# Kernel tuning notes

Hardware: AMD Instinct MI355X
Metric: run time of the kernel (lower is better)

## Reference

```python
import jax, jax.numpy as jnp
import numpy as np

B, H, W = 8, 256, 256
NF = 64          # num_feat
E = 12           # num_expert
D = NF * 4       # token dim = 256
CD = D * E       # expanded dim = 3072


def _lrelu(x):
    return jnp.where(x >= 0, x, 0.2 * x)


def _conv(x, w, stride, pad):
    return jax.lax.conv_general_dilated(
        x, w, (stride, stride), [(pad, pad), (pad, pad)],
        dimension_numbers=('NCHW', 'OIHW', 'NCHW'))


def _bn(x, g, b):
    # training-mode BatchNorm2d: batch statistics over (N, H, W)
    m = jnp.mean(x, axis=(0, 2, 3), keepdims=True)
    v = jnp.var(x, axis=(0, 2, 3), keepdims=True)
    xn = (x - m) * jax.lax.rsqrt(v + 1e-5)
    return xn * g[None, :, None, None] + b[None, :, None, None]


def setup_inputs() -> dict:
    key = jax.random.key(0)
    ks = jax.random.split(key, 16)
    s = 0.05
    d = {}
    d['x'] = jax.random.normal(ks[0], (B, 3, H, W), jnp.float32)
    d['conv0_w'] = jax.random.normal(ks[1], (NF, 3, 3, 3)) * s
    d['conv0_b'] = jnp.zeros((NF,))
    d['conv1_w'] = jax.random.normal(ks[2], (NF, NF, 4, 4)) * s
    d['bn1_g'] = jnp.ones((NF,)); d['bn1_b'] = jnp.zeros((NF,))
    d['conv2_w'] = jax.random.normal(ks[3], (2 * NF, NF, 3, 3)) * s
    d['bn2_g'] = jnp.ones((2 * NF,)); d['bn2_b'] = jnp.zeros((2 * NF,))
    d['conv3_w'] = jax.random.normal(ks[4], (2 * NF, 2 * NF, 4, 4)) * s
    d['bn3_g'] = jnp.ones((2 * NF,)); d['bn3_b'] = jnp.zeros((2 * NF,))
    d['conv4_w'] = jax.random.normal(ks[5], (4 * NF, 2 * NF, 3, 3)) * s
    d['bn4_g'] = jnp.ones((4 * NF,)); d['bn4_b'] = jnp.zeros((4 * NF,))
    d['conv5_w'] = jax.random.normal(ks[6], (4 * NF, 4 * NF, 3, 3)) * s
    d['bn5_g'] = jnp.ones((4 * NF,)); d['bn5_b'] = jnp.zeros((4 * NF,))
    d['conv6_w'] = jax.random.normal(ks[7], (4 * NF, 4 * NF, 3, 3)) * s
    d['bn6_g'] = jnp.ones((4 * NF,)); d['bn6_b'] = jnp.zeros((4 * NF,))
    d['w_gating'] = jax.random.normal(ks[8], (D, E))          # torch.randn init
    d['body_w'] = jax.random.normal(ks[9], (D, CD)) * s       # Linear(c_dim, c_dim*blocks)
    d['body_b'] = jnp.zeros((CD,))
    d['ortho_w'] = jax.random.normal(ks[10], (1, 1, CD))      # OrthorTransform weight
    d['cls_w1'] = jax.random.normal(ks[11], (D, NF // 2)) * s # shared classifier
    d['cls_b1'] = jnp.zeros((NF // 2,))
    d['cls_w2'] = jax.random.normal(ks[12], (NF // 2, 1)) * s
    d['cls_b2'] = jnp.zeros((1,))
    return d


def reference(x, conv0_w, conv0_b, conv1_w, bn1_g, bn1_b, conv2_w, bn2_g, bn2_b,
              conv3_w, bn3_g, bn3_b, conv4_w, bn4_g, bn4_b, conv5_w, bn5_g, bn5_b,
              conv6_w, bn6_g, bn6_b, w_gating, body_w, body_b, ortho_w,
              cls_w1, cls_b1, cls_w2, cls_b2):
    # --- FE conv stack ---
    h = _lrelu(_conv(x, conv0_w, 1, 1) + conv0_b[None, :, None, None])
    h = _lrelu(_bn(_conv(h, conv1_w, 2, 1), bn1_g, bn1_b))
    h = _lrelu(_bn(_conv(h, conv2_w, 1, 1), bn2_g, bn2_b))
    h = _lrelu(_bn(_conv(h, conv3_w, 2, 1), bn3_g, bn3_b))
    h = _lrelu(_bn(_conv(h, conv4_w, 1, 1), bn4_g, bn4_b))
    h = _lrelu(_bn(_conv(h, conv5_w, 1, 1), bn5_g, bn5_b))
    h = _lrelu(_bn(_conv(h, conv6_w, 1, 1), bn6_g, bn6_b))
    b, c, hh, ww = h.shape
    tok = h.reshape(b, c, hh * ww).transpose(0, 2, 1)            # (B, N, D)
    # --- softmax router ---
    routing = jax.nn.softmax(jnp.einsum('bnd,de->bne', tok, w_gating), axis=-1)
    # --- CodeReduction: Linear + lrelu, OrthorTransform multiply, lrelu ---
    feat = _lrelu(tok @ body_w + body_b)                         # (B, N, E*D)
    feat = _lrelu(feat * ortho_w)
    feat = feat.reshape(b, hh * ww, E, D)                        # torch.split chunks
    # --- shared expert MLP on every chunk (all classifiers alias one module) ---
    hid = _lrelu(jnp.einsum('bned,df->bnef', feat, cls_w1) + cls_b1)
    outs = (jnp.einsum('bnef,fo->bneo', hid, cls_w2) + cls_b2)[..., 0]  # (B,N,E)
    # --- top-1 select (equivalent to the torch.where cascade) ---
    idx = jnp.argmax(routing, axis=-1, keepdims=True)
    output = jnp.take_along_axis(outs, idx, axis=-1)             # (B, N, 1)
    return output
```

## Files before the change

### kernel.cpp

```cpp
#include <hip/hip_runtime.h>

__device__ __forceinline__ float lrelu(float x) { return x >= 0.f ? x : 0.2f * x; }

typedef const __attribute__((address_space(1))) void* gas_ptr;
typedef __attribute__((address_space(3))) void* las_ptr;

__global__ __launch_bounds__(256) void conv0_k(const float* __restrict__ x,
                                               const float* __restrict__ w,
                                               const float* __restrict__ bias,
                                               float* __restrict__ out) {
    __shared__ float sIn[3][34][34];
    __shared__ float sW[27][16];
    const int H = 256;
    int tid = threadIdx.x, tx = tid & 31, ty = tid >> 5;
    int tX = (blockIdx.x & 7) * 32, tY = (blockIdx.x >> 3) * 32;
    int b = blockIdx.y, cog = blockIdx.z * 16;
    float acc[4][16] = {};
    const float* inB = x + (size_t)b * 3 * H * H;
    for (int idx = tid; idx < 3 * 1156; idx += 256) {
        int ci = idx / 1156, r = idx % 1156, iy = r / 34, ix = r % 34;
        int gy = tY - 1 + iy, gx = tX - 1 + ix;
        float v = 0.f;
        if ((unsigned)gy < 256u && (unsigned)gx < 256u)
            v = inB[(ci * H + gy) * H + gx];
        sIn[ci][iy][ix] = v;
    }
    for (int idx = tid; idx < 27 * 16; idx += 256) {
        int co = idx & 15, rest = idx >> 4;
        sW[rest][co] = w[(cog + co) * 27 + rest];
    }
    __syncthreads();
#pragma unroll
    for (int ci = 0; ci < 3; ci++)
#pragma unroll
        for (int dy = 0; dy < 3; dy++)
#pragma unroll
            for (int dx = 0; dx < 3; dx++) {
                float a0 = sIn[ci][ty + dy][tx + dx];
                float a1 = sIn[ci][ty + 8 + dy][tx + dx];
                float a2 = sIn[ci][ty + 16 + dy][tx + dx];
                float a3 = sIn[ci][ty + 24 + dy][tx + dx];
                const float* wp = sW[ci * 9 + dy * 3 + dx];
#pragma unroll
                for (int co = 0; co < 16; co++) {
                    float wv = wp[co];
                    acc[0][co] += a0 * wv; acc[1][co] += a1 * wv;
                    acc[2][co] += a2 * wv; acc[3][co] += a3 * wv;
                }
            }
    float* outB = out + (size_t)(b * 64 + cog) * 67080;
#pragma unroll
    for (int co = 0; co < 16; co++) {
        float bv = bias[cog + co];
#pragma unroll
        for (int r = 0; r < 4; r++)
            outB[(size_t)co * 67080 + (size_t)(tY + ty + 8 * r + 1) * 260 +
                 tX + tx + 1] = lrelu(acc[r][co] + bv);
    }
}

template <int COG>
__device__ __forceinline__ void stats_epilogue(float (&acc)[4][COG], float* red,
                                               double2* part, int cog,
                                               int slotBase, int S, int tid) {
#pragma unroll
    for (int c = 0; c < COG; c++) {
        float s = 0.f, q = 0.f;
#pragma unroll
        for (int j = 0; j < 4; j++) { float v = acc[j][c]; s += v; q += v * v; }
        red[c * 256 + tid] = s;
        red[COG * 256 + c * 256 + tid] = q;
    }
    __syncthreads();
    for (int off = 128; off; off >>= 1) {
        if (tid < off) {
#pragma unroll
            for (int c = 0; c < COG; c++) {
                red[c * 256 + tid] += red[c * 256 + tid + off];
                red[COG * 256 + c * 256 + tid] +=
                    red[COG * 256 + c * 256 + tid + off];
            }
        }
        __syncthreads();
    }
    if (tid < COG) {
        int slot = slotBase + blockIdx.y * gridDim.x + blockIdx.x;
        part[(size_t)(cog + tid) * S + slot].x = (double)red[tid * 256];
        part[(size_t)(cog + tid) * S + slot].y =
            (double)red[COG * 256 + tid * 256];
    }
}

template <int COG>
__global__ __launch_bounds__(256) void c4x4p_k(const float* __restrict__ in,
                                               const float* __restrict__ w,
                                               float* __restrict__ out,
                                               double2* __restrict__ part,
                                               int slotBase, int S,
                                               int Cin, int Cout, int Hin,
                                               int Hp, int Wp,
                                               int oHp, int oWp, int oOff) {
    __shared__ float sIn[2][4488];
    __shared__ float sW[2][16 * COG];
    const int Hout = Hin >> 1;
    const int tid = threadIdx.x, tx = tid & 31, ty = tid >> 5;
    const int tpr = Hout >> 5;
    const int tX = (blockIdx.x % tpr) * 32, tY = (blockIdx.x / tpr) * 32;
    const int b = blockIdx.y, cog = blockIdx.z * COG;
    const int HWin = Hp * Wp;
    const float* inB = in + (size_t)b * Cin * HWin;
    const int wvbase = tid & ~63;

    int gOff[5]; int lOff[5]; bool act[5];
#pragma unroll
    for (int r = 0; r < 5; r++) {
        int idx = tid + r * 256;
        bool a = idx < 1122;
        int row = idx / 17, c4 = idx % 17;
        gOff[r] = a ? ((2 * tY + row) * Wp + 2 * tX + 4 * c4) : 0;
        lOff[r] = (r * 256 + wvbase) * 4;
        act[r] = a;
    }
    const int wco = tid % COG, wt = tid / COG;
    const int wgo = ((cog + wco) * Cin) * 16 + wt;
    const bool wact = tid < 16 * COG;

    float acc[4][COG];
#pragma unroll
    for (int j = 0; j < 4; j++)
#pragma unroll
        for (int c = 0; c < COG; c++) acc[j][c] = 0.f;

#pragma unroll
    for (int r = 0; r < 5; r++)
        if (act[r])
            __builtin_amdgcn_global_load_lds((gas_ptr)(inB + gOff[r]),
                                             (las_ptr)(&sIn[0][lOff[r]]), 16, 0, 0);
    if (wact)
        __builtin_amdgcn_global_load_lds((gas_ptr)(w + wgo),
                                         (las_ptr)(&sW[0][wvbase]), 4, 0, 0);
    __syncthreads();

    for (int k = 0; k < Cin; k++) {
        const int cur = k & 1, nb = cur ^ 1;
        const bool more = (k + 1) < Cin;
        if (more) {
            const float* p = inB + (size_t)(k + 1) * HWin;
#pragma unroll
            for (int r = 0; r < 5; r++)
                if (act[r])
                    __builtin_amdgcn_global_load_lds(
                        (gas_ptr)(p + gOff[r]),
                        (las_ptr)(&sIn[nb][lOff[r]]), 16, 0, 0);
            if (wact)
                __builtin_amdgcn_global_load_lds(
                    (gas_ptr)(w + wgo + (k + 1) * 16),
                    (las_ptr)(&sW[nb][wvbase]), 4, 0, 0);
        }
        const float* sI = sIn[cur];
        const float* sw = sW[cur];
#pragma unroll
        for (int dy = 0; dy < 4; dy++)
#pragma unroll
            for (int dx = 0; dx < 4; dx++) {
                const float* bp = sI + (2 * ty + dy) * 68 + 2 * tx + dx;
                float a0 = bp[0];
                float a1 = bp[16 * 68];
                float a2 = bp[32 * 68];
                float a3 = bp[48 * 68];
                const float* wp = sw + (dy * 4 + dx) * COG;
#pragma unroll
                for (int c = 0; c < COG; c++) {
                    float wv = wp[c];
                    acc[0][c] += a0 * wv; acc[1][c] += a1 * wv;
                    acc[2][c] += a2 * wv; acc[3][c] += a3 * wv;
                }
            }
        __syncthreads();
    }

    float* outB = out + (size_t)(b * Cout + cog) * oHp * oWp;
#pragma unroll
    for (int c = 0; c < COG; c++)
#pragma unroll
        for (int r = 0; r < 4; r++)
            outB[(size_t)c * oHp * oWp +
                 (size_t)(tY + ty + 8 * r + oOff) * oWp + tX + tx + oOff] =
                acc[r][c];
    stats_epilogue<COG>(acc, &sIn[0][0], part, cog, slotBase, S, tid);
}

template <int COG>
__global__ __launch_bounds__(256) void c3x3_k(const float* __restrict__ in,
                                              const float* __restrict__ w,
                                              float* __restrict__ out,
                                              double2* __restrict__ part,
                                              int slotBase, int S,
                                              int Cin, int Cout, int H,
                                              int Hp, int Wp,
                                              int oHp, int oWp, int oOff) {
    constexpr int RS = 36;
    constexpr int CI = 34 * RS;
    __shared__ float sIn[2][2 * CI];
    __shared__ float sW[2][18 * COG];
    const int tid = threadIdx.x, tx = tid & 31, ty = tid >> 5;
    const int tpr = H >> 5;
    const int tX = (blockIdx.x % tpr) * 32, tY = (blockIdx.x / tpr) * 32;
    const int b = blockIdx.y, cog = blockIdx.z * COG;
    const int HWin = Hp * Wp;
    const float* inB = in + (size_t)b * Cin * HWin;
    const int wvbase = tid & ~63;

    int gOff[3]; int lOff[3]; bool act[3];
#pragma unroll
    for (int r = 0; r < 3; r++) {
        int idx = tid + r * 256;
        bool a = idx < 612;
        int ci = idx / 306, rem = idx % 306;
        int row = rem / 9, c4 = rem % 9;
        gOff[r] = a ? (ci * HWin + (tY + row) * Wp + tX + 4 * c4) : 0;
        lOff[r] = (r * 256 + wvbase) * 4;
        act[r] = a;
    }
    constexpr int NW = (18 * COG + 255) / 256;
    int wgo[NW]; bool wact[NW];
#pragma unroll
    for (int r = 0; r < NW; r++) {
        int widx = tid + r * 256;
        bool a = widx < 18 * COG;
        int co = widx % COG, rest = widx / COG;
        int ci = rest / 9, t = rest % 9;
        wgo[r] = a ? (((cog + co) * Cin + ci) * 9 + t) : 0;
        wact[r] = a;
    }

    float acc[4][COG];
#pragma unroll
    for (int j = 0; j < 4; j++)
#pragma unroll
        for (int c = 0; c < COG; c++) acc[j][c] = 0.f;

    const int steps = Cin >> 1;

#pragma unroll
    for (int r = 0; r < 3; r++)
        if (act[r])
            __builtin_amdgcn_global_load_lds(
                (gas_ptr)(inB + gOff[r]),
                (las_ptr)(&sIn[0][lOff[r]]), 16, 0, 0);
#pragma unroll
    for (int r = 0; r < NW; r++)
        if (wact[r])
            __builtin_amdgcn_global_load_lds(
                (gas_ptr)(w + wgo[r]),
                (las_ptr)(&sW[0][r * 256 + wvbase]), 4, 0, 0);
    __syncthreads();

    for (int k = 0; k < steps; k++) {
        const int cur = k & 1;
        const int nb = cur ^ 1;
        const bool more = (k + 1) < steps;
        if (more) {
            const int c0n = 2 * (k + 1);
            const float* p = inB + (size_t)c0n * HWin;
            const float* wp2 = w + (size_t)c0n * 9;
#pragma unroll
            for (int r = 0; r < 3; r++)
                if (act[r])
                    __builtin_amdgcn_global_load_lds(
                        (gas_ptr)(p + gOff[r]),
                        (las_ptr)(&sIn[nb][lOff[r]]), 16, 0, 0);
#pragma unroll
            for (int r = 0; r < NW; r++)
                if (wact[r])
                    __builtin_amdgcn_global_load_lds(
                        (gas_ptr)(wp2 + wgo[r]),
                        (las_ptr)(&sW[nb][r * 256 + wvbase]), 4, 0, 0);
        }
        const float* sI = sIn[cur];
        const float* sw = sW[cur];
#pragma unroll
        for (int ci = 0; ci < 2; ci++)
#pragma unroll
            for (int dx = 0; dx < 3; dx++) {
                const float* bp = sI + ci * CI + (4 * ty) * RS + tx + dx;
                float a[6];
#pragma unroll
                for (int j = 0; j < 6; j++) a[j] = bp[j * RS];
#pragma unroll
                for (int dy = 0; dy < 3; dy++) {
                    const float* wp = sw + (ci * 9 + dy * 3 + dx) * COG;
#pragma unroll
                    for (int c = 0; c < COG; c++) {
                        float wv = wp[c];
                        acc[0][c] += a[0 + dy] * wv;
                        acc[1][c] += a[1 + dy] * wv;
                        acc[2][c] += a[2 + dy] * wv;
                        acc[3][c] += a[3 + dy] * wv;
                    }
                }
            }
        __syncthreads();
    }

    float* outB = out + (size_t)(b * Cout + cog) * oHp * oWp;
#pragma unroll
    for (int c = 0; c < COG; c++)
#pragma unroll
        for (int j = 0; j < 4; j++)
            outB[(size_t)c * oHp * oWp +
                 (size_t)(tY + 4 * ty + j + oOff) * oWp + tX + tx + oOff] =
                acc[j][c];
    stats_epilogue<COG>(acc, &sIn[0][0], part, cog, slotBase, S, tid);
}

__global__ void bnfin_k(const double2* __restrict__ part, int S, int C, double invN,
                        const float* __restrict__ g, const float* __restrict__ bb,
                        float2* __restrict__ ss) {
    int c = threadIdx.x;
    if (c >= C) return;
    double sum = 0.0, sq = 0.0;
    for (int s = 0; s < S; s++) {
        double2 p = part[(size_t)c * S + s];
        sum += p.x; sq += p.y;
    }
    double m = sum * invN;
    double v = sq * invN - m * m;
    double sc = (double)g[c] / sqrt(v + 1e-5);
    ss[c] = make_float2((float)sc, (float)((double)bb[c] - m * sc));
}

__global__ __launch_bounds__(256) void bnact_k(float* __restrict__ p,
                                               const float2* __restrict__ ss,
                                               int C, int H, int W,
                                               int Hp, int Wp) {
    int pc = blockIdx.x;
    int c = pc & (C - 1);
    float2 t = ss ? ss[c] : make_float2(1.f, 0.f);
    bool xf = (ss != nullptr);
    float* pl = p + (size_t)pc * Hp * Wp;
    int n = Hp * Wp;
    for (int i = threadIdx.x; i < n; i += 256) {
        int y = i / Wp, x = i - y * Wp;
        bool inter = (y >= 1) && (y <= H) && (x >= 1) && (x <= W);
        if (!inter) pl[i] = 0.f;
        else if (xf) { float v = pl[i]; pl[i] = lrelu(t.x * v + t.y); }
    }
}

__global__ __launch_bounds__(256) void transp_k(const float* __restrict__ h6,
                                                const float2* __restrict__ ss,
                                                float* __restrict__ tok) {
    __shared__ float sT[32][33];
    int tx = threadIdx.x & 31, ty = threadIdx.x >> 5;
    int n0 = blockIdx.x * 32, d0 = blockIdx.y * 32, b = blockIdx.z;
    const float* hb = h6 + ((size_t)b * 256 + d0) * 4096 + n0;
#pragma unroll
    for (int r = 0; r < 4; r++) {
        int d = ty + 8 * r;
        float2 t = ss[d0 + d];
        sT[d][tx] = lrelu(t.x * hb[d * 4096 + tx] + t.y);
    }
    __syncthreads();
    float* tb = tok + ((size_t)b * 4096 + n0) * 256 + d0;
#pragma unroll
    for (int r = 0; r < 4; r++) {
        int n = ty + 8 * r;
        tb[n * 256 + tx] = sT[tx][n];
    }
}

__global__ __launch_bounds__(256) void token_k(const float* __restrict__ tok,
                                               const float* __restrict__ wg,
                                               const float* __restrict__ bw,
                                               const float* __restrict__ bb,
                                               const float* __restrict__ ow,
                                               const float* __restrict__ w1,
                                               const float* __restrict__ b1,
                                               const float* __restrict__ w2,
                                               const float* __restrict__ b2,
                                               float* __restrict__ outp) {
    __shared__ float sf[4][256];
    const int tid = threadIdx.x, wave = tid >> 6, l = tid & 63;
    const int t = blockIdx.x * 4 + wave;
    const float4 tv = reinterpret_cast<const float4*>(tok + (size_t)t * 256)[l];
    sf[wave][4 * l + 0] = tv.x; sf[wave][4 * l + 1] = tv.y;
    sf[wave][4 * l + 2] = tv.z; sf[wave][4 * l + 3] = tv.w;

    float lg[12];
#pragma unroll
    for (int e = 0; e < 12; e++) lg[e] = 0.f;
    const float tj[4] = {tv.x, tv.y, tv.z, tv.w};
#pragma unroll
    for (int j = 0; j < 4; j++) {
        const float* wr = wg + (4 * l + j) * 12;
#pragma unroll
        for (int e = 0; e < 12; e++) lg[e] += tj[j] * wr[e];
    }
#pragma unroll
    for (int off = 32; off > 0; off >>= 1) {
#pragma unroll
        for (int e = 0; e < 12; e++) lg[e] += __shfl_xor(lg[e], off);
    }
    int idx = 0; float best = lg[0];
#pragma unroll
    for (int e = 1; e < 12; e++)
        if (lg[e] > best) { best = lg[e]; idx = e; }
    const int cb = idx * 256;

    float f0 = 0.f, f1 = 0.f, f2 = 0.f, f3 = 0.f;
    const float* bwp = bw + cb + 4 * l;
#pragma unroll 4
    for (int d = 0; d < 256; d++) {
        const float td = sf[wave][d];
        const float4 wv = *reinterpret_cast<const float4*>(bwp + (size_t)d * 3072);
        f0 += td * wv.x; f1 += td * wv.y;
        f2 += td * wv.z; f3 += td * wv.w;
    }
    float fj[4] = {f0, f1, f2, f3};
#pragma unroll
    for (int j = 0; j < 4; j++) {
        int jj = cb + 4 * l + j;
        float v = lrelu(fj[j] + bb[jj]);
        v = lrelu(v * ow[jj]);
        sf[wave][4 * l + j] = v;
    }

    float o = 0.f;
    if (l < 32) {
        float h = b1[l];
#pragma unroll 4
        for (int j = 0; j < 256; j++) h += sf[wave][j] * w1[j * 32 + l];
        h = lrelu(h);
        o = h * w2[l];
    }
    o += __shfl_xor(o, 16); o += __shfl_xor(o, 8); o += __shfl_xor(o, 4);
    o += __shfl_xor(o, 2);  o += __shfl_xor(o, 1);
    if (l == 0) outp[t] = o + b2[0];
}

extern "C" void kernel_launch(void* const* d_in, const int* in_sizes, int n_in,
                              void* d_out, int out_size, void* d_ws, size_t ws_size,
                              hipStream_t stream) {
    const float* x   = (const float*)d_in[0];
    const float* w0  = (const float*)d_in[1];
    const float* b0  = (const float*)d_in[2];
    const float* w1  = (const float*)d_in[3];
    const float* g1  = (const float*)d_in[4];
    const float* be1 = (const float*)d_in[5];
    const float* w2  = (const float*)d_in[6];
    const float* g2  = (const float*)d_in[7];
    const float* be2 = (const float*)d_in[8];
    const float* w3  = (const float*)d_in[9];
    const float* g3  = (const float*)d_in[10];
    const float* be3 = (const float*)d_in[11];
    const float* w4  = (const float*)d_in[12];
    const float* g4  = (const float*)d_in[13];
    const float* be4 = (const float*)d_in[14];
    const float* w5  = (const float*)d_in[15];
    const float* g5  = (const float*)d_in[16];
    const float* be5 = (const float*)d_in[17];
    const float* w6  = (const float*)d_in[18];
    const float* g6  = (const float*)d_in[19];
    const float* be6 = (const float*)d_in[20];
    const float* wg  = (const float*)d_in[21];
    const float* bw  = (const float*)d_in[22];
    const float* bbp = (const float*)d_in[23];
    const float* owp = (const float*)d_in[24];
    const float* cw1 = (const float*)d_in[25];
    const float* cb1 = (const float*)d_in[26];
    const float* cw2 = (const float*)d_in[27];
    const float* cb2 = (const float*)d_in[28];

    char* W = (char*)d_ws;
    float2* ssb = (float2*)W;
    float2* ss1 = ssb;
    float2* ss2 = ssb + 64;
    float2* ss3 = ssb + 192;
    float2* ss4 = ssb + 320;
    float2* ss5 = ssb + 576;
    float2* ss6 = ssb + 832;
    double2* part = (double2*)(W + 16384);

    char* BIG = W + 278528;
    float* h0p = (float*)(BIG);
    float* h1p = (float*)(BIG + 70287360);
    float* h2p = (float*)(BIG);
    float* h3p = (float*)(BIG + 70287360);
    float* h4p = (float*)(BIG);
    float* h5p = (float*)(BIG + 36765696);
    float* h6  = (float*)(BIG);
    float* tok = (float*)(BIG + 36765696);

    bnact_k<<<256, 256, 0, stream>>>(h0p, nullptr, 64, 256, 256, 258, 260);
    for (int half = 0; half < 2; half++) {
        conv0_k<<<dim3(64, 4, 4), 256, 0, stream>>>(
            x + (size_t)half * 4 * 3 * 65536, w0, b0, h0p);
        c4x4p_k<8><<<dim3(16, 4, 8), 256, 0, stream>>>(
            h0p, w1, h1p + (size_t)half * 4 * 64 * 17160, part, half * 64, 128,
            64, 64, 256, 258, 260, 130, 132, 1);
    }
    bnfin_k<<<1, 256, 0, stream>>>(part, 128, 64, 1.0 / 131072.0, g1, be1, ss1);
    bnact_k<<<512, 256, 0, stream>>>(h1p, ss1, 64, 128, 128, 130, 132);
    c3x3_k<8><<<dim3(16, 8, 16), 256, 0, stream>>>(
        h1p, w2, h2p, part, 0, 128, 64, 128, 128, 130, 132, 130, 132, 1);
    bnfin_k<<<1, 256, 0, stream>>>(part, 128, 128, 1.0 / 131072.0, g2, be2, ss2);
    bnact_k<<<1024, 256, 0, stream>>>(h2p, ss2, 128, 128, 128, 130, 132);
    c4x4p_k<8><<<dim3(4, 8, 16), 256, 0, stream>>>(
        h2p, w3, h3p, part, 0, 32, 128, 128, 128, 130, 132, 66, 68, 1);
    bnfin_k<<<1, 256, 0, stream>>>(part, 32, 128, 1.0 / 32768.0, g3, be3, ss3);
    bnact_k<<<1024, 256, 0, stream>>>(h3p, ss3, 128, 64, 64, 66, 68);
    c3x3_k<8><<<dim3(4, 8, 32), 256, 0, stream>>>(
        h3p, w4, h4p, part, 0, 32, 128, 256, 64, 66, 68, 66, 68, 1);
    bnfin_k<<<1, 256, 0, stream>>>(part, 32, 256, 1.0 / 32768.0, g4, be4, ss4);
    bnact_k<<<2048, 256, 0, stream>>>(h4p, ss4, 256, 64, 64, 66, 68);
    c3x3_k<8><<<dim3(4, 8, 32), 256, 0, stream>>>(
        h4p, w5, h5p, part, 0, 32, 256, 256, 64, 66, 68, 66, 68, 1);
    bnfin_k<<<1, 256, 0, stream>>>(part, 32, 256, 1.0 / 32768.0, g5, be5, ss5);
    bnact_k<<<2048, 256, 0, stream>>>(h5p, ss5, 256, 64, 64, 66, 68);
    c3x3_k<8><<<dim3(4, 8, 32), 256, 0, stream>>>(
        h5p, w6, h6, part, 0, 32, 256, 256, 64, 66, 68, 64, 64, 0);
    bnfin_k<<<1, 256, 0, stream>>>(part, 32, 256, 1.0 / 32768.0, g6, be6, ss6);
    transp_k<<<dim3(128, 8, 8), 256, 0, stream>>>(h6, ss6, tok);
    token_k<<<8192, 256, 0, stream>>>(tok, wg, bw, bbp, owp, cw1, cb1, cw2, cb2,
                                      (float*)d_out);
}
```

Before: 2.583 ms.

## Halve conv output tile height and use wave-shuffle BN stats reduction

Conv tiles for the 4x4 strided and 3x3 kernels shrink from 32x32 to 32x16 outputs per block. Each thread now computes 2 rows instead of 4, which doubles the grid and the number of BN partial slots. The shared-memory tree reduction over 256 threads is replaced by a per-wave shuffle reduction followed by a 4-wave sum, which cuts many __syncthreads. The aim is more blocks, lower LDS use and register pressure, and a cheaper epilogue. In exchange, each block reuses fewer loaded inputs and weights, so halo overhead per output rises.

```diff
diff --git a/kernel.cpp b/kernel.cpp
--- a/kernel.cpp
+++ b/kernel.cpp
@@ -60,34 +60,31 @@
 }
 
 template <int COG>
-__device__ __forceinline__ void stats_epilogue(float (&acc)[4][COG], float* red,
-                                               double2* part, int cog,
-                                               int slotBase, int S, int tid) {
+__device__ __forceinline__ void stats_epi(float (&acc)[2][COG],
+                                          float* sRedS, float* sRedQ,
+                                          double2* part, int cog,
+                                          int slotBase, int S, int tid) {
+    const int wv = tid >> 6, l = tid & 63;
 #pragma unroll
     for (int c = 0; c < COG; c++) {
-        float s = 0.f, q = 0.f;
-#pragma unroll
-        for (int j = 0; j < 4; j++) { float v = acc[j][c]; s += v; q += v * v; }
-        red[c * 256 + tid] = s;
-        red[COG * 256 + c * 256 + tid] = q;
+        float s = acc[0][c] + acc[1][c];
+        float q = acc[0][c] * acc[0][c] + acc[1][c] * acc[1][c];
+#pragma unroll
+        for (int off = 32; off > 0; off >>= 1) {
+            s += __shfl_xor(s, off);
+            q += __shfl_xor(q, off);
+        }
+        if (l == 0) { sRedS[wv * COG + c] = s; sRedQ[wv * COG + c] = q; }
     }
     __syncthreads();
-    for (int off = 128; off; off >>= 1) {
-        if (tid < off) {
-#pragma unroll
-            for (int c = 0; c < COG; c++) {
-                red[c * 256 + tid] += red[c * 256 + tid + off];
-                red[COG * 256 + c * 256 + tid] +=
-                    red[COG * 256 + c * 256 + tid + off];
-            }
-        }
-        __syncthreads();
-    }
     if (tid < COG) {
+        float s = sRedS[tid] + sRedS[COG + tid] + sRedS[2 * COG + tid] +
+                  sRedS[3 * COG + tid];
+        float q = sRedQ[tid] + sRedQ[COG + tid] + sRedQ[2 * COG + tid] +
+                  sRedQ[3 * COG + tid];
         int slot = slotBase + blockIdx.y * gridDim.x + blockIdx.x;
-        part[(size_t)(cog + tid) * S + slot].x = (double)red[tid * 256];
-        part[(size_t)(cog + tid) * S + slot].y =
-            (double)red[COG * 256 + tid * 256];
+        part[(size_t)(cog + tid) * S + slot].x = (double)s;
+        part[(size_t)(cog + tid) * S + slot].y = (double)q;
     }
 }
 
@@ -100,22 +97,23 @@
                                                int Cin, int Cout, int Hin,
                                                int Hp, int Wp,
                                                int oHp, int oWp, int oOff) {
-    __shared__ float sIn[2][4488];
+    __shared__ float sIn[2][2312];
     __shared__ float sW[2][16 * COG];
+    __shared__ float sRedS[4 * COG], sRedQ[4 * COG];
     const int Hout = Hin >> 1;
     const int tid = threadIdx.x, tx = tid & 31, ty = tid >> 5;
     const int tpr = Hout >> 5;
-    const int tX = (blockIdx.x % tpr) * 32, tY = (blockIdx.x / tpr) * 32;
+    const int tX = (blockIdx.x % tpr) * 32, tY = (blockIdx.x / tpr) * 16;
     const int b = blockIdx.y, cog = blockIdx.z * COG;
     const int HWin = Hp * Wp;
     const float* inB = in + (size_t)b * Cin * HWin;
     const int wvbase = tid & ~63;
 
-    int gOff[5]; int lOff[5]; bool act[5];
-#pragma unroll
-    for (int r = 0; r < 5; r++) {
+    int gOff[3]; int lOff[3]; bool act[3];
+#pragma unroll
+    for (int r = 0; r < 3; r++) {
         int idx = tid + r * 256;
-        bool a = idx < 1122;
+        bool a = idx < 578;
         int row = idx / 17, c4 = idx % 17;
         gOff[r] = a ? ((2 * tY + row) * Wp + 2 * tX + 4 * c4) : 0;
         lOff[r] = (r * 256 + wvbase) * 4;
@@ -125,14 +123,14 @@
     const int wgo = ((cog + wco) * Cin) * 16 + wt;
     const bool wact = tid < 16 * COG;
 
-    float acc[4][COG];
-#pragma unroll
-    for (int j = 0; j < 4; j++)
+    float acc[2][COG];
+#pragma unroll
+    for (int j = 0; j < 2; j++)
 #pragma unroll
         for (int c = 0; c < COG; c++) acc[j][c] = 0.f;
 
 #pragma unroll
-    for (int r = 0; r < 5; r++)
+    for (int r = 0; r < 3; r++)
         if (act[r])
             __builtin_amdgcn_global_load_lds((gas_ptr)(inB + gOff[r]),
                                              (las_ptr)(&sIn[0][lOff[r]]), 16, 0, 0);
@@ -147,7 +145,7 @@
         if (more) {
             const float* p = inB + (size_t)(k + 1) * HWin;
 #pragma unroll
-            for (int r = 0; r < 5; r++)
+            for (int r = 0; r < 3; r++)
                 if (act[r])
                     __builtin_amdgcn_global_load_lds(
                         (gas_ptr)(p + gOff[r]),
@@ -163,17 +161,14 @@
         for (int dy = 0; dy < 4; dy++)
 #pragma unroll
             for (int dx = 0; dx < 4; dx++) {
-                const float* bp = sI + (2 * ty + dy) * 68 + 2 * tx + dx;
+                const float* bp = sI + (4 * ty + dy) * 68 + 2 * tx + dx;
                 float a0 = bp[0];
-                float a1 = bp[16 * 68];
-                float a2 = bp[32 * 68];
-                float a3 = bp[48 * 68];
+                float a1 = bp[2 * 68];
                 const float* wp = sw + (dy * 4 + dx) * COG;
 #pragma unroll
                 for (int c = 0; c < COG; c++) {
                     float wv = wp[c];
                     acc[0][c] += a0 * wv; acc[1][c] += a1 * wv;
-                    acc[2][c] += a2 * wv; acc[3][c] += a3 * wv;
                 }
             }
         __syncthreads();
@@ -183,11 +178,11 @@
 #pragma unroll
     for (int c = 0; c < COG; c++)
 #pragma unroll
-        for (int r = 0; r < 4; r++)
+        for (int j = 0; j < 2; j++)
             outB[(size_t)c * oHp * oWp +
-                 (size_t)(tY + ty + 8 * r + oOff) * oWp + tX + tx + oOff] =
-                acc[r][c];
-    stats_epilogue<COG>(acc, &sIn[0][0], part, cog, slotBase, S, tid);
+                 (size_t)(tY + 2 * ty + j + oOff) * oWp + tX + tx + oOff] =
+                acc[j][c];
+    stats_epi<COG>(acc, sRedS, sRedQ, part, cog, slotBase, S, tid);
 }
 
 template <int COG>
@@ -200,23 +195,24 @@
                                               int Hp, int Wp,
                                               int oHp, int oWp, int oOff) {
     constexpr int RS = 36;
-    constexpr int CI = 34 * RS;
+    constexpr int CI = 18 * RS;
     __shared__ float sIn[2][2 * CI];
     __shared__ float sW[2][18 * COG];
+    __shared__ float sRedS[4 * COG], sRedQ[4 * COG];
     const int tid = threadIdx.x, tx = tid & 31, ty = tid >> 5;
     const int tpr = H >> 5;
-    const int tX = (blockIdx.x % tpr) * 32, tY = (blockIdx.x / tpr) * 32;
+    const int tX = (blockIdx.x % tpr) * 32, tY = (blockIdx.x / tpr) * 16;
     const int b = blockIdx.y, cog = blockIdx.z * COG;
     const int HWin = Hp * Wp;
     const float* inB = in + (size_t)b * Cin * HWin;
     const int wvbase = tid & ~63;
 
-    int gOff[3]; int lOff[3]; bool act[3];
-#pragma unroll
-    for (int r = 0; r < 3; r++) {
+    int gOff[2]; int lOff[2]; bool act[2];
+#pragma unroll
+    for (int r = 0; r < 2; r++) {
         int idx = tid + r * 256;
-        bool a = idx < 612;
-        int ci = idx / 306, rem = idx % 306;
+        bool a = idx < 324;
+        int ci = idx / 162, rem = idx % 162;
         int row = rem / 9, c4 = rem % 9;
         gOff[r] = a ? (ci * HWin + (tY + row) * Wp + tX + 4 * c4) : 0;
         lOff[r] = (r * 256 + wvbase) * 4;
@@ -234,16 +230,16 @@
         wact[r] = a;
     }
 
-    float acc[4][COG];
-#pragma unroll
-    for (int j = 0; j < 4; j++)
+    float acc[2][COG];
+#pragma unroll
+    for (int j = 0; j < 2; j++)
 #pragma unroll
         for (int c = 0; c < COG; c++) acc[j][c] = 0.f;
 
     const int steps = Cin >> 1;
 
 #pragma unroll
-    for (int r = 0; r < 3; r++)
+    for (int r = 0; r < 2; r++)
         if (act[r])
             __builtin_amdgcn_global_load_lds(
                 (gas_ptr)(inB + gOff[r]),
@@ -265,7 +261,7 @@
             const float* p = inB + (size_t)c0n * HWin;
             const float* wp2 = w + (size_t)c0n * 9;
 #pragma unroll
-            for (int r = 0; r < 3; r++)
+            for (int r = 0; r < 2; r++)
                 if (act[r])
                     __builtin_amdgcn_global_load_lds(
                         (gas_ptr)(p + gOff[r]),
@@ -283,10 +279,10 @@
         for (int ci = 0; ci < 2; ci++)
 #pragma unroll
             for (int dx = 0; dx < 3; dx++) {
-                const float* bp = sI + ci * CI + (4 * ty) * RS + tx + dx;
-                float a[6];
-#pragma unroll
-                for (int j = 0; j < 6; j++) a[j] = bp[j * RS];
+                const float* bp = sI + ci * CI + (2 * ty) * RS + tx + dx;
+                float a[4];
+#pragma unroll
+                for (int j = 0; j < 4; j++) a[j] = bp[j * RS];
 #pragma unroll
                 for (int dy = 0; dy < 3; dy++) {
                     const float* wp = sw + (ci * 9 + dy * 3 + dx) * COG;
@@ -295,8 +291,6 @@
                         float wv = wp[c];
                         acc[0][c] += a[0 + dy] * wv;
                         acc[1][c] += a[1 + dy] * wv;
-                        acc[2][c] += a[2 + dy] * wv;
-                        acc[3][c] += a[3 + dy] * wv;
                     }
                 }
             }
@@ -307,11 +301,11 @@
 #pragma unroll
     for (int c = 0; c < COG; c++)
 #pragma unroll
-        for (int j = 0; j < 4; j++)
+        for (int j = 0; j < 2; j++)
             outB[(size_t)c * oHp * oWp +
-                 (size_t)(tY + 4 * ty + j + oOff) * oWp + tX + tx + oOff] =
+                 (size_t)(tY + 2 * ty + j + oOff) * oWp + tX + tx + oOff] =
                 acc[j][c];
-    stats_epilogue<COG>(acc, &sIn[0][0], part, cog, slotBase, S, tid);
+    stats_epi<COG>(acc, sRedS, sRedQ, part, cog, slotBase, S, tid);
 }
 
 __global__ void bnfin_k(const double2* __restrict__ part, int S, int C, double invN,
@@ -482,7 +476,7 @@
     float2* ss6 = ssb + 832;
     double2* part = (double2*)(W + 16384);
 
-    char* BIG = W + 278528;
+    char* BIG = W + 540672;
     float* h0p = (float*)(BIG);
     float* h1p = (float*)(BIG + 70287360);
     float* h2p = (float*)(BIG);
@@ -496,31 +490,31 @@
     for (int half = 0; half < 2; half++) {
         conv0_k<<<dim3(64, 4, 4), 256, 0, stream>>>(
             x + (size_t)half * 4 * 3 * 65536, w0, b0, h0p);
-        c4x4p_k<8><<<dim3(16, 4, 8), 256, 0, stream>>>(
-            h0p, w1, h1p + (size_t)half * 4 * 64 * 17160, part, half * 64, 128,
+        c4x4p_k<8><<<dim3(32, 4, 8), 256, 0, stream>>>(
+            h0p, w1, h1p + (size_t)half * 4 * 64 * 17160, part, half * 128, 256,
             64, 64, 256, 258, 260, 130, 132, 1);
     }
-    bnfin_k<<<1, 256, 0, stream>>>(part, 128, 64, 1.0 / 131072.0, g1, be1, ss1);
+    bnfin_k<<<1, 256, 0, stream>>>(part, 256, 64, 1.0 / 131072.0, g1, be1, ss1);
     bnact_k<<<512, 256, 0, stream>>>(h1p, ss1, 64, 128, 128, 130, 132);
-    c3x3_k<8><<<dim3(16, 8, 16), 256, 0, stream>>>(
-        h1p, w2, h2p, part, 0, 128, 64, 128, 128, 130, 132, 130, 132, 1);
-    bnfin_k<<<1, 256, 0, stream>>>(part, 128, 128, 1.0 / 131072.0, g2, be2, ss2);
+    c3x3_k<8><<<dim3(32, 8, 16), 256, 0, stream>>>(
+        h1p, w2, h2p, part, 0, 256, 64, 128, 128, 130, 132, 130, 132, 1);
+    bnfin_k<<<1, 256, 0, stream>>>(part, 256, 128, 1.0 / 131072.0, g2, be2, ss2);
     bnact_k<<<1024, 256, 0, stream>>>(h2p, ss2, 128, 128, 128, 130, 132);
-    c4x4p_k<8><<<dim3(4, 8, 16), 256, 0, stream>>>(
-        h2p, w3, h3p, part, 0, 32, 128, 128, 128, 130, 132, 66, 68, 1);
-    bnfin_k<<<1, 256, 0, stream>>>(part, 32, 128, 1.0 / 32768.0, g3, be3, ss3);
+    c4x4p_k<8><<<dim3(8, 8, 16), 256, 0, stream>>>(
+        h2p, w3, h3p, part, 0, 64, 128, 128, 128, 130, 132, 66, 68, 1);
+    bnfin_k<<<1, 256, 0, stream>>>(part, 64, 128, 1.0 / 32768.0, g3, be3, ss3);
     bnact_k<<<1024, 256, 0, stream>>>(h3p, ss3, 128, 64, 64, 66, 68);
-    c3x3_k<8><<<dim3(4, 8, 32), 256, 0, stream>>>(
-        h3p, w4, h4p, part, 0, 32, 128, 256, 64, 66, 68, 66, 68, 1);
-    bnfin_k<<<1, 256, 0, stream>>>(part, 32, 256, 1.0 / 32768.0, g4, be4, ss4);
+    c3x3_k<8><<<dim3(8, 8, 32), 256, 0, stream>>>(
+        h3p, w4, h4p, part, 0, 64, 128, 256, 64, 66, 68, 66, 68, 1);
+    bnfin_k<<<1, 256, 0, stream>>>(part, 64, 256, 1.0 / 32768.0, g4, be4, ss4);
     bnact_k<<<2048, 256, 0, stream>>>(h4p, ss4, 256, 64, 64, 66, 68);
-    c3x3_k<8><<<dim3(4, 8, 32), 256, 0, stream>>>(
-        h4p, w5, h5p, part, 0, 32, 256, 256, 64, 66, 68, 66, 68, 1);
-    bnfin_k<<<1, 256, 0, stream>>>(part, 32, 256, 1.0 / 32768.0, g5, be5, ss5);
+    c3x3_k<8><<<dim3(8, 8, 32), 256, 0, stream>>>(
+        h4p, w5, h5p, part, 0, 64, 256, 256, 64, 66, 68, 66, 68, 1);
+    bnfin_k<<<1, 256, 0, stream>>>(part, 64, 256, 1.0 / 32768.0, g5, be5, ss5);
     bnact_k<<<2048, 256, 0, stream>>>(h5p, ss5, 256, 64, 64, 66, 68);
-    c3x3_k<8><<<dim3(4, 8, 32), 256, 0, stream>>>(
-        h5p, w6, h6, part, 0, 32, 256, 256, 64, 66, 68, 64, 64, 0);
-    bnfin_k<<<1, 256, 0, stream>>>(part, 32, 256, 1.0 / 32768.0, g6, be6, ss6);
+    c3x3_k<8><<<dim3(8, 8, 32), 256, 0, stream>>>(
+        h5p, w6, h6, part, 0, 64, 256, 256, 64, 66, 68, 64, 64, 0);
+    bnfin_k<<<1, 256, 0, stream>>>(part, 64, 256, 1.0 / 32768.0, g6, be6, ss6);
     transp_k<<<dim3(128, 8, 8), 256, 0, stream>>>(h6, ss6, tok);
     token_k<<<8192, 256, 0, stream>>>(tok, wg, bw, bbp, owp, cw1, cb1, cw2, cb2,
                                       (float*)d_out);
```

Measured after the change: 2.860 ms. +10.7%, slower.
